# Kernel tuning notes

Measured on AMD Instinct MI355X. Metric: run time of the kernel, lower is better.

## Reference

```python
import jax, jax.numpy as jnp
import numpy as np

P_EPS = 1e-6            # nn.PairwiseDistance default eps
ALPHA = 0.25
STD_TARGET = 1.0
NUM_COMMUNITIES = 512   # C = number of unique community ids
BIG = 1e30              # masking value for hard-negative min


def setup_inputs() -> dict:
    key = jax.random.key(0)
    k1, k2, k3 = jax.random.split(key, 3)
    B, N, D, C = 1, 100000, 128, NUM_COMMUNITIES
    node_features = jax.random.normal(k1, (B, N, D), dtype=jnp.float32)
    # row 0: a permutation of node indices; row 1: community of that node.
    perm = jax.random.permutation(k2, N).astype(jnp.int32)
    comm_per_node = jnp.concatenate([
        jnp.arange(C, dtype=jnp.int32),  # guarantee every community appears
        jax.random.randint(k3, (N - C,), 0, C, dtype=jnp.int32),
    ])
    community_belong_list = jnp.stack([perm, comm_per_node[perm]])  # [2, N]
    return {"node_features": node_features, "community_belong_list": community_belong_list}


def reference(node_features, community_belong_list):
    B, N, D = node_features.shape
    C = NUM_COMMUNITIES
    dt = node_features.dtype

    # ---- _community_inverse_permute: invert row-0 permutation, reorder columns ----
    perm = community_belong_list[0]
    inv = jnp.zeros((N,), perm.dtype).at[perm].add(jnp.arange(N, dtype=perm.dtype))
    cbl = community_belong_list[:, inv]          # row0 == arange(N) after this
    comm = cbl[1]                                # [N] community id per node
    src = node_features[:, cbl[0], :]            # [B,N,D] gather (identity order)

    # ---- groupby sum / count -> community means ----
    comm_sum = jnp.zeros((B, C, D), dt).at[:, comm, :].add(src)        # [B,C,D]
    counts = jnp.zeros((C,), dt).at[comm].add(jnp.asarray(1.0, dt))   # [C]
    comm_mean = comm_sum / counts[None, :, None]                      # [B,C,D]

    # ---- cdist(node_features, comm_mean, p=2) -> [B,N,C] ----
    x2 = jnp.sum(node_features * node_features, -1)                   # [B,N]
    c2 = jnp.sum(comm_mean * comm_mean, -1)                           # [B,C]
    dots = jnp.einsum('bnd,bcd->bnc', node_features, comm_mean)
    distance = jnp.sqrt(jnp.maximum(x2[:, :, None] + c2[:, None, :] - 2.0 * dots, 0.0))

    # ---- leave-one-out community mean per node, positive distance ----
    cnt_pn = counts[comm]                                             # [N]
    cnt_m1 = jnp.maximum(cnt_pn - 1.0, 1.0)                           # [N]
    x_minus = jnp.where((cnt_pn == 1.0)[None, :, None], jnp.asarray(0.0, dt), src)
    loo_mean = (comm_sum[:, comm, :] - x_minus) / cnt_m1[None, :, None]
    pos_dist = jnp.sqrt(jnp.sum((loo_mean - src + P_EPS) ** 2, -1))   # [B,N]

    # ---- negatives: all communities except the node's own ----
    own = distance[:, jnp.arange(N), comm]                            # [B,N]
    mean_neg = (jnp.sum(distance, -1) - own) / (C - 1)                # [B,N]
    pos_mask = jnp.zeros((N, C), bool).at[jnp.arange(N), comm].set(True)
    hard_neg = jnp.min(jnp.where(pos_mask[None], jnp.asarray(BIG, dt), distance), -1)

    trip_mean = jnp.maximum(pos_dist - mean_neg + ALPHA, 0.0)
    trip_min = jnp.maximum(pos_dist - hard_neg + ALPHA, 0.0)

    # ---- groupby std (unbiased) per community per feature ----
    sq = jnp.zeros((B, C, D), dt).at[:, comm, :].add((src - comm_mean[:, comm, :]) ** 2)
    std = jnp.sqrt(sq / jnp.maximum(counts - 1.0, 1.0)[None, :, None])

    return (trip_mean.mean(), trip_min.mean(), ((std - STD_TARGET) ** 2).mean())
```

## Files before the change

### kernel.cpp

```cpp
#include <hip/hip_runtime.h>

#define NCOMM 512
#define DIM   128
#define ALPHA 0.25f
#define PEPS  1e-6f
#define BIGF  1e30f
#define TILE_C 16
#define NT    (NCOMM / TILE_C)

typedef __attribute__((ext_vector_type(8))) short bf16x8;
typedef __attribute__((ext_vector_type(4))) float f32x4;

__device__ __forceinline__ unsigned short bf16_rn(float v) {
    unsigned u = __float_as_uint(v);
    u += 0x7FFFu + ((u >> 16) & 1u);
    return (unsigned short)(u >> 16);
}
__device__ __forceinline__ float bf16_f(unsigned short h) {
    return __uint_as_float((unsigned)h << 16);
}

#define GLOAD_LDS16(g, l) __builtin_amdgcn_global_load_lds( \
    (const __attribute__((address_space(1))) void*)(g), \
    (__attribute__((address_space(3))) void*)(l), 16, 0, 0)


__global__ void k_inv(const int* __restrict__ cbl, int* __restrict__ inv, int N) {
    int i = blockIdx.x * 256 + threadIdx.x;
    if (i < N) inv[cbl[i]] = i;
}

__global__ void k_comm(const int* __restrict__ cbl, const int* __restrict__ inv,
                       int* __restrict__ comm, int* __restrict__ idx0,
                       int* __restrict__ counts, int N) {
    __shared__ int h[NCOMM];
    int t = threadIdx.x;
    h[t] = 0; h[t + 256] = 0;
    __syncthreads();
    int j = blockIdx.x * 256 + t;
    if (j < N) {
        int ij = inv[j];
        int c  = cbl[N + ij];
        comm[j] = c;
        idx0[j] = cbl[ij];
        atomicAdd(&h[c], 1);
    }
    __syncthreads();
    int v = h[t];        if (v) atomicAdd(&counts[t], v);
    v = h[t + 256];      if (v) atomicAdd(&counts[t + 256], v);
}

__global__ void k_scan(const int* __restrict__ counts, int* __restrict__ offsets,
                       int* __restrict__ cursor, float* __restrict__ countf) {
    __shared__ int sc[NCOMM];
    int t = threadIdx.x;
    int v0 = counts[t];
    sc[t] = v0;
    __syncthreads();
    for (int off = 1; off < NCOMM; off <<= 1) {
        int v = (t >= off) ? sc[t - off] : 0;
        __syncthreads();
        sc[t] += v;
        __syncthreads();
    }
    int excl = sc[t] - v0;
    offsets[t] = excl;
    cursor[t]  = excl;
    countf[t]  = (float)v0;
}

__global__ void k_sort(const int* __restrict__ comm, int* __restrict__ cursor,
                       int* __restrict__ sorted, int N) {
    __shared__ int h[NCOMM], hb[NCOMM];
    int t = threadIdx.x;
    h[t] = 0; h[t + 256] = 0;
    __syncthreads();
    int j0 = blockIdx.x * 1024 + t;
    int cs[4];
    #pragma unroll
    for (int q = 0; q < 4; ++q) {
        int j = j0 + q * 256;
        cs[q] = (j < N) ? comm[j] : -1;
        if (cs[q] >= 0) atomicAdd(&h[cs[q]], 1);
    }
    __syncthreads();
    int v = h[t];        if (v) hb[t] = atomicAdd(&cursor[t], v);
    v = h[t + 256];      if (v) hb[t + 256] = atomicAdd(&cursor[t + 256], v);
    __syncthreads();
    #pragma unroll
    for (int q = 0; q < 4; ++q) {
        int j = j0 + q * 256;
        if (cs[q] >= 0) {
            int p = atomicAdd(&hb[cs[q]], 1);
            sorted[p] = j;
        }
    }
}


__global__ void __launch_bounds__(256) k_stats(
        const float* __restrict__ NF, const int* __restrict__ idx0,
        const int* __restrict__ sorted, const int* __restrict__ offsets,
        const int* __restrict__ counts,
        float* __restrict__ comm_sum,
        unsigned short* __restrict__ CMh, unsigned short* __restrict__ CMl,
        float* __restrict__ c2, float* __restrict__ accum) {
    __shared__ int ridx[512];
    __shared__ float4 bufS[256], bufQ[256];
    int c = blockIdx.x, t = threadIdx.x;
    int d4 = t & 31, r = t >> 5;
    int cnt = counts[c], base = offsets[c];
    const float4* NF4 = (const float4*)NF;

    float4 s4 = make_float4(0.f, 0.f, 0.f, 0.f);
    float4 q4 = make_float4(0.f, 0.f, 0.f, 0.f);
    for (int chunk = 0; chunk < cnt; chunk += 512) {
        int m = min(cnt - chunk, 512);
        for (int i = t; i < m; i += 256) ridx[i] = idx0[sorted[base + chunk + i]];
        __syncthreads();
        for (int i = r; i < m; i += 8) {
            float4 v = NF4[(size_t)ridx[i] * 32 + d4];
            s4.x += v.x; s4.y += v.y; s4.z += v.z; s4.w += v.w;
            q4.x = fmaf(v.x, v.x, q4.x); q4.y = fmaf(v.y, v.y, q4.y);
            q4.z = fmaf(v.z, v.z, q4.z); q4.w = fmaf(v.w, v.w, q4.w);
        }
        __syncthreads();
    }
    bufS[t] = s4; bufQ[t] = q4;
    __syncthreads();
    if (t < 128) {
        float4 a = bufS[t], b = bufS[t + 128];
        a.x += b.x; a.y += b.y; a.z += b.z; a.w += b.w; bufS[t] = a;
        float4 e = bufQ[t], f = bufQ[t + 128];
        e.x += f.x; e.y += f.y; e.z += f.z; e.w += f.w; bufQ[t] = e;
    }
    __syncthreads();
    if (t < 64) {
        float4 a = bufS[t], b = bufS[t + 64];
        a.x += b.x; a.y += b.y; a.z += b.z; a.w += b.w; bufS[t] = a;
        float4 e = bufQ[t], f = bufQ[t + 64];
        e.x += f.x; e.y += f.y; e.z += f.z; e.w += f.w; bufQ[t] = e;
    }
    __syncthreads();
    if (t < 32) {
        float4 a = bufS[t], b = bufS[t + 32];
        a.x += b.x; a.y += b.y; a.z += b.z; a.w += b.w;
        float4 e = bufQ[t], f = bufQ[t + 32];
        e.x += f.x; e.y += f.y; e.z += f.z; e.w += f.w;
        float sarr[4] = {a.x, a.y, a.z, a.w};
        float qarr[4] = {e.x, e.y, e.z, e.w};
        float cf = (float)cnt;
        float mm = 0.f, ee = 0.f;
        #pragma unroll
        for (int k = 0; k < 4; ++k) {
            int d = t * 4 + k;
            float s = sarr[k];
            comm_sum[c * DIM + d] = s;
            float m = (cnt > 0) ? s / cf : 0.f;
            unsigned short h = bf16_rn(m);
            CMh[c * DIM + d] = h;
            CMl[c * DIM + d] = bf16_rn(m - bf16_f(h));
            float varn = fmaxf(fmaf(-cf * m, m, qarr[k]), 0.f);
            float stdv = sqrtf(varn / fmaxf(cf - 1.f, 1.f));
            float er = stdv - 1.f;
            mm = fmaf(m, m, mm);
            ee = fmaf(er, er, ee);
        }
        #pragma unroll
        for (int msk = 1; msk < 32; msk <<= 1) {
            mm += __shfl_xor(mm, msk);
            ee += __shfl_xor(ee, msk);
        }
        if (t == 0) {
            c2[c] = mm;
            atomicAdd(&accum[2], ee);
        }
    }
}


__global__ void __launch_bounds__(256, 2) k_main(
        const float* __restrict__ NF,
        const unsigned short* __restrict__ CMh,
        const unsigned short* __restrict__ CMl,
        const float* __restrict__ comm_sum,
        const float* __restrict__ c2g,
        const float* __restrict__ countf,
        const int* __restrict__ comm,
        const int* __restrict__ idx0,
        float* __restrict__ accum, int N) {
    __shared__ unsigned short Bst[4][2][2][TILE_C * DIM];
    __shared__ float c2s[NCOMM];
    __shared__ int   comms[128];
    __shared__ float x2s[128];
    __shared__ float sums[128], mins[128];
    __shared__ float red[8];

    int tid = threadIdx.x;
    int w  = tid >> 6;
    int l  = tid & 63;
    int lr = l & 15;
    int lk = l >> 4;
    int n0 = blockIdx.x * 128;

    auto stage = [&](int tt, int b) {
        int c0 = tt * TILE_C;
        unsigned short* lh = &Bst[w][b][0][0];
        unsigned short* ll = &Bst[w][b][1][0];
        #pragma unroll
        for (int i = 0; i < 4; ++i) {
            int p = i * 64 + l;
            int row = p >> 4, cp = p & 15;
            size_t gch = ((size_t)(c0 + row) * 16 + (cp ^ row)) * 8;
            GLOAD_LDS16(CMh + gch, lh + i * 512);
            GLOAD_LDS16(CMl + gch, ll + i * 512);
        }
    };
    stage(0, 0);

    c2s[tid]       = c2g[tid];
    c2s[tid + 256] = c2g[tid + 256];
    if (tid < 128) {
        int gn = n0 + tid;
        comms[tid] = (gn < N) ? comm[gn] : -1;
    }

    bf16x8 ah[2][4], al[2][4];
    #pragma unroll
    for (int mf = 0; mf < 2; ++mf) {
        int n = n0 + w * 32 + mf * 16 + lr;
        const float4* src = (const float4*)NF + (size_t)n * 32 + lk * 2;
        float p2 = 0.f;
        #pragma unroll
        for (int ks = 0; ks < 4; ++ks) {
            float4 v0 = make_float4(0.f, 0.f, 0.f, 0.f), v1 = v0;
            if (n < N) { v0 = src[ks * 8]; v1 = src[ks * 8 + 1]; }
            float fr[8] = {v0.x, v0.y, v0.z, v0.w, v1.x, v1.y, v1.z, v1.w};
            bf16x8 hh, ll;
            #pragma unroll
            for (int t = 0; t < 8; ++t) {
                unsigned short h = bf16_rn(fr[t]);
                hh[t] = (short)h;
                ll[t] = (short)bf16_rn(fr[t] - bf16_f(h));
                p2 = fmaf(fr[t], fr[t], p2);
            }
            ah[mf][ks] = hh; al[mf][ks] = ll;
        }
        p2 += __shfl_xor(p2, 16);
        p2 += __shfl_xor(p2, 32);
        if (lk == 0) x2s[w * 32 + mf * 16 + lr] = p2;
    }
    __syncthreads();

    float x2v[2][4], sumv[2][4], minv[2][4];
    int cnv[2][4];
    #pragma unroll
    for (int mf = 0; mf < 2; ++mf)
        #pragma unroll
        for (int j = 0; j < 4; ++j) {
            int idx = w * 32 + mf * 16 + lk * 4 + j;
            x2v[mf][j] = x2s[idx];
            cnv[mf][j] = comms[idx];
            sumv[mf][j] = 0.f; minv[mf][j] = BIGF;
        }

    int buf = 0;
    for (int tt = 0; tt < NT; ++tt) {
        if (tt + 1 < NT) {
            stage(tt + 1, buf ^ 1);
            asm volatile("s_waitcnt vmcnt(8)" ::: "memory");
        } else {
            asm volatile("s_waitcnt vmcnt(0)" ::: "memory");
        }
        __builtin_amdgcn_sched_barrier(0);

        const unsigned short* bhp = &Bst[w][buf][0][0];
        const unsigned short* blp = &Bst[w][buf][1][0];
        f32x4 ae0 = {0.f, 0.f, 0.f, 0.f}, ao0 = ae0, ae1 = ae0, ao1 = ae0;
        #pragma unroll
        for (int hf = 0; hf < 2; ++hf) {
            int ke = hf * 2, ko = hf * 2 + 1;
            int che = (ke * 4 + lk) ^ lr;
            int cho = (ko * 4 + lk) ^ lr;
            bf16x8 bhe = *(const bf16x8*)&bhp[(lr * 16 + che) * 8];
            bf16x8 bho = *(const bf16x8*)&bhp[(lr * 16 + cho) * 8];
            bf16x8 ble = *(const bf16x8*)&blp[(lr * 16 + che) * 8];
            bf16x8 blo = *(const bf16x8*)&blp[(lr * 16 + cho) * 8];
            ae0 = __builtin_amdgcn_mfma_f32_16x16x32_bf16(ah[0][ke], bhe, ae0, 0, 0, 0);
            ae1 = __builtin_amdgcn_mfma_f32_16x16x32_bf16(ah[1][ke], bhe, ae1, 0, 0, 0);
            ao0 = __builtin_amdgcn_mfma_f32_16x16x32_bf16(ah[0][ko], bho, ao0, 0, 0, 0);
            ao1 = __builtin_amdgcn_mfma_f32_16x16x32_bf16(ah[1][ko], bho, ao1, 0, 0, 0);
            ae0 = __builtin_amdgcn_mfma_f32_16x16x32_bf16(al[0][ke], bhe, ae0, 0, 0, 0);
            ae1 = __builtin_amdgcn_mfma_f32_16x16x32_bf16(al[1][ke], bhe, ae1, 0, 0, 0);
            ao0 = __builtin_amdgcn_mfma_f32_16x16x32_bf16(al[0][ko], bho, ao0, 0, 0, 0);
            ao1 = __builtin_amdgcn_mfma_f32_16x16x32_bf16(al[1][ko], bho, ao1, 0, 0, 0);
            ae0 = __builtin_amdgcn_mfma_f32_16x16x32_bf16(ah[0][ke], ble, ae0, 0, 0, 0);
            ae1 = __builtin_amdgcn_mfma_f32_16x16x32_bf16(ah[1][ke], ble, ae1, 0, 0, 0);
            ao0 = __builtin_amdgcn_mfma_f32_16x16x32_bf16(ah[0][ko], blo, ao0, 0, 0, 0);
            ao1 = __builtin_amdgcn_mfma_f32_16x16x32_bf16(ah[1][ko], blo, ao1, 0, 0, 0);
        }
        f32x4 acc0 = ae0 + ao0;
        f32x4 acc1 = ae1 + ao1;
        int ccol = tt * TILE_C + lr;
        float c2v = c2s[ccol];
        #pragma unroll
        for (int j = 0; j < 4; ++j) {
            float d2a = fmaf(-2.f, acc0[j], x2v[0][j] + c2v);
            float da  = __builtin_amdgcn_sqrtf(fmaxf(d2a, 0.f));
            sumv[0][j] += da;
            minv[0][j] = fminf(minv[0][j], (cnv[0][j] == ccol) ? BIGF : da);
            float d2b = fmaf(-2.f, acc1[j], x2v[1][j] + c2v);
            float db  = __builtin_amdgcn_sqrtf(fmaxf(d2b, 0.f));
            sumv[1][j] += db;
            minv[1][j] = fminf(minv[1][j], (cnv[1][j] == ccol) ? BIGF : db);
        }
        buf ^= 1;
    }

    #pragma unroll
    for (int mf = 0; mf < 2; ++mf)
        #pragma unroll
        for (int j = 0; j < 4; ++j) {
            float sv = sumv[mf][j], mv = minv[mf][j];
            #pragma unroll
            for (int msk = 1; msk < 16; msk <<= 1) {
                sv += __shfl_xor(sv, msk);
                mv = fminf(mv, __shfl_xor(mv, msk));
            }
            if (lr == 0) {
                int idx = w * 32 + mf * 16 + lk * 4 + j;
                sums[idx] = sv; mins[idx] = mv;
            }
        }
    __syncthreads();

    float tmean = 0.f, tminv = 0.f;
    {
        int ln = tid >> 1, half = tid & 1;
        int n = n0 + ln;
        if (n < N) {
            int cnode = comms[ln];
            float cf  = countf[cnode];
            float cm1 = fmaxf(cf - 1.f, 1.f);
            float rs  = 1.f / cm1;
            bool single = (cf == 1.f);
            const float4* srow = (const float4*)(NF + (size_t)idx0[n] * DIM) + half * 16;
            const float4* csum = (const float4*)(comm_sum + (size_t)cnode * DIM) + half * 16;
            float q = 0.f, dot = 0.f;
            #pragma unroll
            for (int m = 0; m < 16; ++m) {
                float4 sv = srow[m];
                float4 cs = csum[m];
                float4 xm = single ? make_float4(0.f, 0.f, 0.f, 0.f) : sv;
                float lx = (cs.x - xm.x) * rs - sv.x + PEPS;
                float ly = (cs.y - xm.y) * rs - sv.y + PEPS;
                float lz = (cs.z - xm.z) * rs - sv.z + PEPS;
                float lw = (cs.w - xm.w) * rs - sv.w + PEPS;
                q = fmaf(lx, lx, fmaf(ly, ly, fmaf(lz, lz, fmaf(lw, lw, q))));
                dot = fmaf(sv.x, cs.x, fmaf(sv.y, cs.y, fmaf(sv.z, cs.z, fmaf(sv.w, cs.w, dot))));
            }
            q   += __shfl_xor(q, 1);
            dot += __shfl_xor(dot, 1);
            if (half == 0) {
                float pos = sqrtf(q);
                float ownd2 = x2s[ln] + c2s[cnode] - 2.f * (dot / cf);
                float own = sqrtf(fmaxf(ownd2, 0.f));
                float mean_neg = (sums[ln] - own) * (1.f / (float)(NCOMM - 1));
                tmean = fmaxf(pos - mean_neg + ALPHA, 0.f);
                tminv = fmaxf(pos - mins[ln] + ALPHA, 0.f);
            }
        }
    }
    #pragma unroll
    for (int msk = 1; msk < 64; msk <<= 1) {
        tmean += __shfl_xor(tmean, msk);
        tminv += __shfl_xor(tminv, msk);
    }
    if ((tid & 63) == 0) { red[w * 2] = tmean; red[w * 2 + 1] = tminv; }
    __syncthreads();
    if (tid == 0) {
        atomicAdd(&accum[0], red[0] + red[2] + red[4] + red[6]);
        atomicAdd(&accum[1], red[1] + red[3] + red[5] + red[7]);
    }
}

__global__ void k_final(const float* __restrict__ accum, float* __restrict__ out, int N) {
    if (threadIdx.x == 0) {
        out[0] = accum[0] / (float)N;
        out[1] = accum[1] / (float)N;
        out[2] = accum[2] / (float)(NCOMM * DIM);
    }
}


extern "C" void kernel_launch(void* const* d_in, const int* in_sizes, int n_in,
                              void* d_out, int out_size, void* d_ws, size_t ws_size,
                              hipStream_t stream) {
    const float* NF  = (const float*)d_in[0];
    const int*   CBL = (const int*)d_in[1];
    int N = in_sizes[1] / 2;
    if (N <= 0) return;

    char* ws = (char*)d_ws;
    float* accum   = (float*)ws;
    int*   counts  = (int*)(ws + 16);
    int*   cursor  = (int*)(ws + 16 + 2048);
    int*   offsets = (int*)(ws + 16 + 2 * 2048);
    float* countf  = (float*)(ws + 16 + 3 * 2048);
    float* c2      = (float*)(ws + 16 + 4 * 2048);
    char* p = ws + 16 + 5 * 2048;
    int* inv    = (int*)p; p += (size_t)N * 4;
    int* comm   = (int*)p; p += (size_t)N * 4;
    int* idx0   = (int*)p; p += (size_t)N * 4;
    int* sorted = (int*)p; p += (size_t)N * 4;
    float* comm_sum = (float*)p; p += (size_t)NCOMM * DIM * 4;
    unsigned short* CMh = (unsigned short*)p; p += (size_t)NCOMM * DIM * 2;
    unsigned short* CMl = (unsigned short*)p;

    hipMemsetAsync(d_ws, 0, 16 + 2048, stream);

    int nb = (N + 255) / 256;
    k_inv <<<nb, 256, 0, stream>>>(CBL, inv, N);
    k_comm<<<nb, 256, 0, stream>>>(CBL, inv, comm, idx0, counts, N);
    k_scan<<<1, NCOMM, 0, stream>>>(counts, offsets, cursor, countf);
    int nb4 = (N + 1023) / 1024;
    k_sort<<<nb4, 256, 0, stream>>>(comm, cursor, sorted, N);
    k_stats<<<NCOMM, 256, 0, stream>>>(NF, idx0, sorted, offsets, counts,
                                       comm_sum, CMh, CMl, c2, accum);
    int mb = (N + 127) / 128;
    k_main<<<mb, 256, 0, stream>>>(NF, CMh, CMl, comm_sum, c2, countf,
                                   comm, idx0, accum, N);
    k_final<<<1, 64, 0, stream>>>(accum, (float*)d_out, N);
}
```

Baseline: 147.3 us.

## Split community dimension across two blocks with shared LDS staging and a separate triplet reduction

k_main now splits the 512 communities into two halves, each handled by its own block, which doubles the grid. Partial sums and mins go to global buffers, and a new k_trip kernel combines them and reduces the triplet losses. The B tiles are now shared by all four waves through one double-buffered LDS tile of 32 communities, with __syncthreads, instead of each wave keeping its own copy. This cuts LDS use and lets launch bounds rise to 4 blocks per SM for more occupancy. The cost is the node A-fragments being loaded and converted twice, extra global traffic and a kernel launch, and added block-wide barriers.

After: 223.8 us. 1.52x slower.

```diff
diff --git a/kernel.cpp b/kernel.cpp
--- a/kernel.cpp
+++ b/kernel.cpp
@@ -5,8 +5,7 @@
 #define ALPHA 0.25f
 #define PEPS  1e-6f
 #define BIGF  1e30f
-#define TILE_C 16
-#define NT    (NCOMM / TILE_C)
+#define TILE_C 32
 
 typedef __attribute__((ext_vector_type(8))) short bf16x8;
 typedef __attribute__((ext_vector_type(4))) float f32x4;
@@ -179,7 +178,7 @@
 }
 
 
-__global__ void __launch_bounds__(256, 2) k_main(
+__global__ void __launch_bounds__(256, 4) k_main(
         const float* __restrict__ NF,
         const unsigned short* __restrict__ CMh,
         const unsigned short* __restrict__ CMl,
@@ -188,38 +187,47 @@
         const float* __restrict__ countf,
         const int* __restrict__ comm,
         const int* __restrict__ idx0,
-        float* __restrict__ accum, int N) {
-    __shared__ unsigned short Bst[4][2][2][TILE_C * DIM];
-    __shared__ float c2s[NCOMM];
+        float* __restrict__ sp, float* __restrict__ mp,
+        float* __restrict__ pos_g, float* __restrict__ own_g,
+        int N, int RB) {
+    __shared__ unsigned short Bst[2][2][TILE_C * DIM];
+    __shared__ float c2s[256];
     __shared__ int   comms[128];
     __shared__ float x2s[128];
     __shared__ float sums[128], mins[128];
-    __shared__ float red[8];
 
     int tid = threadIdx.x;
+    int bid = blockIdx.x;
+    int ch  = (bid >= RB) ? 1 : 0;
+    int rb  = bid - ch * RB;
     int w  = tid >> 6;
     int l  = tid & 63;
     int lr = l & 15;
     int lk = l >> 4;
-    int n0 = blockIdx.x * 128;
-
-    auto stage = [&](int tt, int b) {
-        int c0 = tt * TILE_C;
-        unsigned short* lh = &Bst[w][b][0][0];
-        unsigned short* ll = &Bst[w][b][1][0];
-        #pragma unroll
-        for (int i = 0; i < 4; ++i) {
-            int p = i * 64 + l;
-            int row = p >> 4, cp = p & 15;
-            size_t gch = ((size_t)(c0 + row) * 16 + (cp ^ row)) * 8;
-            GLOAD_LDS16(CMh + gch, lh + i * 512);
-            GLOAD_LDS16(CMl + gch, ll + i * 512);
-        }
+    int n0 = rb * 128;
+    int c0 = ch * 256;
+    int NP = RB * 128;
+
+    const unsigned short* pH0; const unsigned short* pH1;
+    const unsigned short* pL0; const unsigned short* pL1;
+    {
+        int r0 = tid >> 4;
+        int s0 = (tid & 15) ^ (r0 & 15);
+        pH0 = CMh + ((size_t)(c0 + r0) * 16 + s0) * 8;
+        pH1 = CMh + ((size_t)(c0 + 16 + r0) * 16 + s0) * 8;
+        pL0 = CMl + ((size_t)(c0 + r0) * 16 + s0) * 8;
+        pL1 = CMl + ((size_t)(c0 + 16 + r0) * 16 + s0) * 8;
+    }
+    auto stage = [&](int b) {
+        GLOAD_LDS16(pH0, &Bst[b][0][(size_t)(0 * 256 + w * 64) * 8]);
+        GLOAD_LDS16(pH1, &Bst[b][0][(size_t)(1 * 256 + w * 64) * 8]);
+        GLOAD_LDS16(pL0, &Bst[b][1][(size_t)(0 * 256 + w * 64) * 8]);
+        GLOAD_LDS16(pL1, &Bst[b][1][(size_t)(1 * 256 + w * 64) * 8]);
+        pH0 += 4096; pH1 += 4096; pL0 += 4096; pL1 += 4096;
     };
-    stage(0, 0);
-
-    c2s[tid]       = c2g[tid];
-    c2s[tid + 256] = c2g[tid + 256];
+    stage(0);
+
+    c2s[tid] = c2g[c0 + tid];
     if (tid < 128) {
         int gn = n0 + tid;
         comms[tid] = (gn < N) ? comm[gn] : -1;
@@ -265,55 +273,55 @@
         }
 
     int buf = 0;
-    for (int tt = 0; tt < NT; ++tt) {
-        if (tt + 1 < NT) {
-            stage(tt + 1, buf ^ 1);
-            asm volatile("s_waitcnt vmcnt(8)" ::: "memory");
-        } else {
-            asm volatile("s_waitcnt vmcnt(0)" ::: "memory");
-        }
-        __builtin_amdgcn_sched_barrier(0);
-
-        const unsigned short* bhp = &Bst[w][buf][0][0];
-        const unsigned short* blp = &Bst[w][buf][1][0];
-        f32x4 ae0 = {0.f, 0.f, 0.f, 0.f}, ao0 = ae0, ae1 = ae0, ao1 = ae0;
-        #pragma unroll
-        for (int hf = 0; hf < 2; ++hf) {
-            int ke = hf * 2, ko = hf * 2 + 1;
-            int che = (ke * 4 + lk) ^ lr;
-            int cho = (ko * 4 + lk) ^ lr;
-            bf16x8 bhe = *(const bf16x8*)&bhp[(lr * 16 + che) * 8];
-            bf16x8 bho = *(const bf16x8*)&bhp[(lr * 16 + cho) * 8];
-            bf16x8 ble = *(const bf16x8*)&blp[(lr * 16 + che) * 8];
-            bf16x8 blo = *(const bf16x8*)&blp[(lr * 16 + cho) * 8];
-            ae0 = __builtin_amdgcn_mfma_f32_16x16x32_bf16(ah[0][ke], bhe, ae0, 0, 0, 0);
-            ae1 = __builtin_amdgcn_mfma_f32_16x16x32_bf16(ah[1][ke], bhe, ae1, 0, 0, 0);
-            ao0 = __builtin_amdgcn_mfma_f32_16x16x32_bf16(ah[0][ko], bho, ao0, 0, 0, 0);
-            ao1 = __builtin_amdgcn_mfma_f32_16x16x32_bf16(ah[1][ko], bho, ao1, 0, 0, 0);
-            ae0 = __builtin_amdgcn_mfma_f32_16x16x32_bf16(al[0][ke], bhe, ae0, 0, 0, 0);
-            ae1 = __builtin_amdgcn_mfma_f32_16x16x32_bf16(al[1][ke], bhe, ae1, 0, 0, 0);
-            ao0 = __builtin_amdgcn_mfma_f32_16x16x32_bf16(al[0][ko], bho, ao0, 0, 0, 0);
-            ao1 = __builtin_amdgcn_mfma_f32_16x16x32_bf16(al[1][ko], bho, ao1, 0, 0, 0);
-            ae0 = __builtin_amdgcn_mfma_f32_16x16x32_bf16(ah[0][ke], ble, ae0, 0, 0, 0);
-            ae1 = __builtin_amdgcn_mfma_f32_16x16x32_bf16(ah[1][ke], ble, ae1, 0, 0, 0);
-            ao0 = __builtin_amdgcn_mfma_f32_16x16x32_bf16(ah[0][ko], blo, ao0, 0, 0, 0);
-            ao1 = __builtin_amdgcn_mfma_f32_16x16x32_bf16(ah[1][ko], blo, ao1, 0, 0, 0);
-        }
-        f32x4 acc0 = ae0 + ao0;
-        f32x4 acc1 = ae1 + ao1;
-        int ccol = tt * TILE_C + lr;
-        float c2v = c2s[ccol];
-        #pragma unroll
-        for (int j = 0; j < 4; ++j) {
-            float d2a = fmaf(-2.f, acc0[j], x2v[0][j] + c2v);
-            float da  = __builtin_amdgcn_sqrtf(fmaxf(d2a, 0.f));
-            sumv[0][j] += da;
-            minv[0][j] = fminf(minv[0][j], (cnv[0][j] == ccol) ? BIGF : da);
-            float d2b = fmaf(-2.f, acc1[j], x2v[1][j] + c2v);
-            float db  = __builtin_amdgcn_sqrtf(fmaxf(d2b, 0.f));
-            sumv[1][j] += db;
-            minv[1][j] = fminf(minv[1][j], (cnv[1][j] == ccol) ? BIGF : db);
-        }
+    for (int tt = 0; tt < 8; ++tt) {
+        if (tt < 7) stage(buf ^ 1);
+
+        #pragma unroll
+        for (int s = 0; s < 2; ++s) {
+            int rbase = s * 16 + lr;
+            const unsigned short* bhp = &Bst[buf][0][0];
+            const unsigned short* blp = &Bst[buf][1][0];
+            f32x4 ae0 = {0.f, 0.f, 0.f, 0.f}, ao0 = ae0, ae1 = ae0, ao1 = ae0;
+            #pragma unroll
+            for (int hf = 0; hf < 2; ++hf) {
+                int ke = hf * 2, ko = hf * 2 + 1;
+                int che = (ke * 4 + lk) ^ lr;
+                int cho = (ko * 4 + lk) ^ lr;
+                bf16x8 bhe = *(const bf16x8*)&bhp[(size_t)(rbase * 16 + che) * 8];
+                bf16x8 bho = *(const bf16x8*)&bhp[(size_t)(rbase * 16 + cho) * 8];
+                bf16x8 ble = *(const bf16x8*)&blp[(size_t)(rbase * 16 + che) * 8];
+                bf16x8 blo = *(const bf16x8*)&blp[(size_t)(rbase * 16 + cho) * 8];
+                ae0 = __builtin_amdgcn_mfma_f32_16x16x32_bf16(ah[0][ke], bhe, ae0, 0, 0, 0);
+                ae1 = __builtin_amdgcn_mfma_f32_16x16x32_bf16(ah[1][ke], bhe, ae1, 0, 0, 0);
+                ao0 = __builtin_amdgcn_mfma_f32_16x16x32_bf16(ah[0][ko], bho, ao0, 0, 0, 0);
+                ao1 = __builtin_amdgcn_mfma_f32_16x16x32_bf16(ah[1][ko], bho, ao1, 0, 0, 0);
+                ae0 = __builtin_amdgcn_mfma_f32_16x16x32_bf16(al[0][ke], bhe, ae0, 0, 0, 0);
+                ae1 = __builtin_amdgcn_mfma_f32_16x16x32_bf16(al[1][ke], bhe, ae1, 0, 0, 0);
+                ao0 = __builtin_amdgcn_mfma_f32_16x16x32_bf16(al[0][ko], bho, ao0, 0, 0, 0);
+                ao1 = __builtin_amdgcn_mfma_f32_16x16x32_bf16(al[1][ko], bho, ao1, 0, 0, 0);
+                ae0 = __builtin_amdgcn_mfma_f32_16x16x32_bf16(ah[0][ke], ble, ae0, 0, 0, 0);
+                ae1 = __builtin_amdgcn_mfma_f32_16x16x32_bf16(ah[1][ke], ble, ae1, 0, 0, 0);
+                ao0 = __builtin_amdgcn_mfma_f32_16x16x32_bf16(ah[0][ko], blo, ao0, 0, 0, 0);
+                ao1 = __builtin_amdgcn_mfma_f32_16x16x32_bf16(ah[1][ko], blo, ao1, 0, 0, 0);
+            }
+            f32x4 acc0 = ae0 + ao0;
+            f32x4 acc1 = ae1 + ao1;
+            int ccl = tt * TILE_C + s * 16 + lr;
+            int ccol = c0 + ccl;
+            float c2v = c2s[ccl];
+            #pragma unroll
+            for (int j = 0; j < 4; ++j) {
+                float d2a = fmaf(-2.f, acc0[j], x2v[0][j] + c2v);
+                float da  = __builtin_amdgcn_sqrtf(fmaxf(d2a, 0.f));
+                sumv[0][j] += da;
+                minv[0][j] = fminf(minv[0][j], (cnv[0][j] == ccol) ? BIGF : da);
+                float d2b = fmaf(-2.f, acc1[j], x2v[1][j] + c2v);
+                float db  = __builtin_amdgcn_sqrtf(fmaxf(d2b, 0.f));
+                sumv[1][j] += db;
+                minv[1][j] = fminf(minv[1][j], (cnv[1][j] == ccol) ? BIGF : db);
+            }
+        }
+        __syncthreads();
         buf ^= 1;
     }
 
@@ -334,8 +342,13 @@
         }
     __syncthreads();
 
-    float tmean = 0.f, tminv = 0.f;
-    {
+    if (tid < 128) {
+        int n = n0 + tid;
+        sp[(size_t)ch * NP + n] = sums[tid];
+        mp[(size_t)ch * NP + n] = mins[tid];
+    }
+
+    if (ch == 0) {
         int ln = tid >> 1, half = tid & 1;
         int n = n0 + ln;
         if (n < N) {
@@ -362,23 +375,39 @@
             q   += __shfl_xor(q, 1);
             dot += __shfl_xor(dot, 1);
             if (half == 0) {
-                float pos = sqrtf(q);
-                float ownd2 = x2s[ln] + c2s[cnode] - 2.f * (dot / cf);
-                float own = sqrtf(fmaxf(ownd2, 0.f));
-                float mean_neg = (sums[ln] - own) * (1.f / (float)(NCOMM - 1));
-                tmean = fmaxf(pos - mean_neg + ALPHA, 0.f);
-                tminv = fmaxf(pos - mins[ln] + ALPHA, 0.f);
-            }
-        }
+                pos_g[n] = sqrtf(q);
+                float ownd2 = x2s[ln] + c2g[cnode] - 2.f * (dot / cf);
+                own_g[n] = sqrtf(fmaxf(ownd2, 0.f));
+            }
+        }
+    }
+}
+
+
+__global__ void __launch_bounds__(256) k_trip(
+        const float* __restrict__ sp, const float* __restrict__ mp,
+        const float* __restrict__ pos_g, const float* __restrict__ own_g,
+        float* __restrict__ accum, int N, int NP) {
+    __shared__ float red[8];
+    int i = blockIdx.x * 256 + threadIdx.x;
+    float tm = 0.f, tn = 0.f;
+    if (i < N) {
+        float own = own_g[i];
+        float sum = sp[i] + sp[(size_t)NP + i] - own;
+        float mn  = fminf(mp[i], mp[(size_t)NP + i]);
+        float pos = pos_g[i];
+        tm = fmaxf(pos - sum * (1.f / (float)(NCOMM - 1)) + ALPHA, 0.f);
+        tn = fmaxf(pos - mn + ALPHA, 0.f);
     }
     #pragma unroll
     for (int msk = 1; msk < 64; msk <<= 1) {
-        tmean += __shfl_xor(tmean, msk);
-        tminv += __shfl_xor(tminv, msk);
-    }
-    if ((tid & 63) == 0) { red[w * 2] = tmean; red[w * 2 + 1] = tminv; }
-    __syncthreads();
-    if (tid == 0) {
+        tm += __shfl_xor(tm, msk);
+        tn += __shfl_xor(tn, msk);
+    }
+    int wv = threadIdx.x >> 6;
+    if ((threadIdx.x & 63) == 0) { red[wv * 2] = tm; red[wv * 2 + 1] = tn; }
+    __syncthreads();
+    if (threadIdx.x == 0) {
         atomicAdd(&accum[0], red[0] + red[2] + red[4] + red[6]);
         atomicAdd(&accum[1], red[1] + red[3] + red[5] + red[7]);
     }
@@ -400,6 +429,8 @@
     const int*   CBL = (const int*)d_in[1];
     int N = in_sizes[1] / 2;
     if (N <= 0) return;
+    int RB = (N + 127) / 128;
+    int NP = RB * 128;
 
     char* ws = (char*)d_ws;
     float* accum   = (float*)ws;
@@ -415,7 +446,11 @@
     int* sorted = (int*)p; p += (size_t)N * 4;
     float* comm_sum = (float*)p; p += (size_t)NCOMM * DIM * 4;
     unsigned short* CMh = (unsigned short*)p; p += (size_t)NCOMM * DIM * 2;
-    unsigned short* CMl = (unsigned short*)p;
+    unsigned short* CMl = (unsigned short*)p; p += (size_t)NCOMM * DIM * 2;
+    float* sp    = (float*)p; p += (size_t)2 * NP * 4;
+    float* mp    = (float*)p; p += (size_t)2 * NP * 4;
+    float* pos_g = (float*)p; p += (size_t)NP * 4;
+    float* own_g = (float*)p;
 
     hipMemsetAsync(d_ws, 0, 16 + 2048, stream);
 
@@ -427,8 +462,8 @@
     k_sort<<<nb4, 256, 0, stream>>>(comm, cursor, sorted, N);
     k_stats<<<NCOMM, 256, 0, stream>>>(NF, idx0, sorted, offsets, counts,
                                        comm_sum, CMh, CMl, c2, accum);
-    int mb = (N + 127) / 128;
-    k_main<<<mb, 256, 0, stream>>>(NF, CMh, CMl, comm_sum, c2, countf,
-                                   comm, idx0, accum, N);
+    k_main<<<2 * RB, 256, 0, stream>>>(NF, CMh, CMl, comm_sum, c2, countf,
+                                       comm, idx0, sp, mp, pos_g, own_g, N, RB);
+    k_trip<<<(N + 255) / 256, 256, 0, stream>>>(sp, mp, pos_g, own_g, accum, N, NP);
     k_final<<<1, 64, 0, stream>>>(accum, (float*)d_out, N);
 }
```

## Process 256 nodes per block and seed MFMA accumulators with x2 term

Applied to the files above, without the earlier changes.

Each wave now handles 64 node rows (four 16-row fragments) instead of 32, so every staged community tile in LDS is reused across twice as many MFMAs. Accumulators start at -0.5*|x|^2, which folds the x2 add into the matrix multiply, and the global staging offsets are precomputed once. The epilogue now uses one thread per node instead of two. The cost is higher register pressure from the larger A fragments and accumulators, and half as many blocks, which could hurt occupancy and load balance.

Measured after the change: 148.4 us. No clear change (+0.8%).

```diff
diff --git a/kernel.cpp b/kernel.cpp
--- a/kernel.cpp
+++ b/kernel.cpp
@@ -191,9 +191,9 @@
         float* __restrict__ accum, int N) {
     __shared__ unsigned short Bst[4][2][2][TILE_C * DIM];
     __shared__ float c2s[NCOMM];
-    __shared__ int   comms[128];
-    __shared__ float x2s[128];
-    __shared__ float sums[128], mins[128];
+    __shared__ int   comms[256];
+    __shared__ float x2s[256];
+    __shared__ float sums[256], mins[256];
     __shared__ float red[8];
 
     int tid = threadIdx.x;
@@ -201,34 +201,38 @@
     int l  = tid & 63;
     int lr = l & 15;
     int lk = l >> 4;
-    int n0 = blockIdx.x * 128;
-
+    int n0 = blockIdx.x * 256;
+
+    int goff[4];
+    #pragma unroll
+    for (int i = 0; i < 4; ++i) {
+        int p = i * 64 + l;
+        int row = p >> 4, cp = p & 15;
+        goff[i] = (row * 16 + (cp ^ row)) * 8;
+    }
     auto stage = [&](int tt, int b) {
-        int c0 = tt * TILE_C;
+        int base = tt * (TILE_C * DIM);
         unsigned short* lh = &Bst[w][b][0][0];
         unsigned short* ll = &Bst[w][b][1][0];
         #pragma unroll
         for (int i = 0; i < 4; ++i) {
-            int p = i * 64 + l;
-            int row = p >> 4, cp = p & 15;
-            size_t gch = ((size_t)(c0 + row) * 16 + (cp ^ row)) * 8;
-            GLOAD_LDS16(CMh + gch, lh + i * 512);
-            GLOAD_LDS16(CMl + gch, ll + i * 512);
+            GLOAD_LDS16(CMh + base + goff[i], lh + i * 512);
+            GLOAD_LDS16(CMl + base + goff[i], ll + i * 512);
         }
     };
     stage(0, 0);
 
     c2s[tid]       = c2g[tid];
     c2s[tid + 256] = c2g[tid + 256];
-    if (tid < 128) {
+    {
         int gn = n0 + tid;
         comms[tid] = (gn < N) ? comm[gn] : -1;
     }
 
-    bf16x8 ah[2][4], al[2][4];
-    #pragma unroll
-    for (int mf = 0; mf < 2; ++mf) {
-        int n = n0 + w * 32 + mf * 16 + lr;
+    bf16x8 ah[4][4], al[4][4];
+    #pragma unroll
+    for (int mf = 0; mf < 4; ++mf) {
+        int n = n0 + w * 64 + mf * 16 + lr;
         const float4* src = (const float4*)NF + (size_t)n * 32 + lk * 2;
         float p2 = 0.f;
         #pragma unroll
@@ -248,19 +252,17 @@
         }
         p2 += __shfl_xor(p2, 16);
         p2 += __shfl_xor(p2, 32);
-        if (lk == 0) x2s[w * 32 + mf * 16 + lr] = p2;
-    }
-    __syncthreads();
-
-    float x2v[2][4], sumv[2][4], minv[2][4];
-    int cnv[2][4];
-    #pragma unroll
-    for (int mf = 0; mf < 2; ++mf)
+        if (lk == 0) x2s[w * 64 + mf * 16 + lr] = -0.5f * p2;
+    }
+    __syncthreads();
+
+    int cnv[4][4];
+    float sumv[4][4], minv[4][4];
+    #pragma unroll
+    for (int mf = 0; mf < 4; ++mf)
         #pragma unroll
         for (int j = 0; j < 4; ++j) {
-            int idx = w * 32 + mf * 16 + lk * 4 + j;
-            x2v[mf][j] = x2s[idx];
-            cnv[mf][j] = comms[idx];
+            cnv[mf][j] = comms[w * 64 + mf * 16 + lk * 4 + j];
             sumv[mf][j] = 0.f; minv[mf][j] = BIGF;
         }
 
@@ -276,49 +278,47 @@
 
         const unsigned short* bhp = &Bst[w][buf][0][0];
         const unsigned short* blp = &Bst[w][buf][1][0];
-        f32x4 ae0 = {0.f, 0.f, 0.f, 0.f}, ao0 = ae0, ae1 = ae0, ao1 = ae0;
-        #pragma unroll
-        for (int hf = 0; hf < 2; ++hf) {
-            int ke = hf * 2, ko = hf * 2 + 1;
-            int che = (ke * 4 + lk) ^ lr;
-            int cho = (ko * 4 + lk) ^ lr;
-            bf16x8 bhe = *(const bf16x8*)&bhp[(lr * 16 + che) * 8];
-            bf16x8 bho = *(const bf16x8*)&bhp[(lr * 16 + cho) * 8];
-            bf16x8 ble = *(const bf16x8*)&blp[(lr * 16 + che) * 8];
-            bf16x8 blo = *(const bf16x8*)&blp[(lr * 16 + cho) * 8];
-            ae0 = __builtin_amdgcn_mfma_f32_16x16x32_bf16(ah[0][ke], bhe, ae0, 0, 0, 0);
-            ae1 = __builtin_amdgcn_mfma_f32_16x16x32_bf16(ah[1][ke], bhe, ae1, 0, 0, 0);
-            ao0 = __builtin_amdgcn_mfma_f32_16x16x32_bf16(ah[0][ko], bho, ao0, 0, 0, 0);
-            ao1 = __builtin_amdgcn_mfma_f32_16x16x32_bf16(ah[1][ko], bho, ao1, 0, 0, 0);
-            ae0 = __builtin_amdgcn_mfma_f32_16x16x32_bf16(al[0][ke], bhe, ae0, 0, 0, 0);
-            ae1 = __builtin_amdgcn_mfma_f32_16x16x32_bf16(al[1][ke], bhe, ae1, 0, 0, 0);
-            ao0 = __builtin_amdgcn_mfma_f32_16x16x32_bf16(al[0][ko], bho, ao0, 0, 0, 0);
-            ao1 = __builtin_amdgcn_mfma_f32_16x16x32_bf16(al[1][ko], bho, ao1, 0, 0, 0);
-            ae0 = __builtin_amdgcn_mfma_f32_16x16x32_bf16(ah[0][ke], ble, ae0, 0, 0, 0);
-            ae1 = __builtin_amdgcn_mfma_f32_16x16x32_bf16(ah[1][ke], ble, ae1, 0, 0, 0);
-            ao0 = __builtin_amdgcn_mfma_f32_16x16x32_bf16(ah[0][ko], blo, ao0, 0, 0, 0);
-            ao1 = __builtin_amdgcn_mfma_f32_16x16x32_bf16(ah[1][ko], blo, ao1, 0, 0, 0);
-        }
-        f32x4 acc0 = ae0 + ao0;
-        f32x4 acc1 = ae1 + ao1;
+        bf16x8 bh[4], bl[4];
+        #pragma unroll
+        for (int ks = 0; ks < 4; ++ks) {
+            int ch = (ks * 4 + lk) ^ lr;
+            bh[ks] = *(const bf16x8*)&bhp[(size_t)(lr * 16 + ch) * 8];
+            bl[ks] = *(const bf16x8*)&blp[(size_t)(lr * 16 + ch) * 8];
+        }
+        f32x4 acc[4];
+        #pragma unroll
+        for (int mf = 0; mf < 4; ++mf)
+            acc[mf] = *(const f32x4*)&x2s[w * 64 + mf * 16 + lk * 4];
+
+        #pragma unroll
+        for (int ks = 0; ks < 4; ++ks) {
+            #pragma unroll
+            for (int mf = 0; mf < 4; ++mf)
+                acc[mf] = __builtin_amdgcn_mfma_f32_16x16x32_bf16(ah[mf][ks], bh[ks], acc[mf], 0, 0, 0);
+            #pragma unroll
+            for (int mf = 0; mf < 4; ++mf)
+                acc[mf] = __builtin_amdgcn_mfma_f32_16x16x32_bf16(al[mf][ks], bh[ks], acc[mf], 0, 0, 0);
+            #pragma unroll
+            for (int mf = 0; mf < 4; ++mf)
+                acc[mf] = __builtin_amdgcn_mfma_f32_16x16x32_bf16(ah[mf][ks], bl[ks], acc[mf], 0, 0, 0);
+        }
+
         int ccol = tt * TILE_C + lr;
         float c2v = c2s[ccol];
         #pragma unroll
-        for (int j = 0; j < 4; ++j) {
-            float d2a = fmaf(-2.f, acc0[j], x2v[0][j] + c2v);
-            float da  = __builtin_amdgcn_sqrtf(fmaxf(d2a, 0.f));
-            sumv[0][j] += da;
-            minv[0][j] = fminf(minv[0][j], (cnv[0][j] == ccol) ? BIGF : da);
-            float d2b = fmaf(-2.f, acc1[j], x2v[1][j] + c2v);
-            float db  = __builtin_amdgcn_sqrtf(fmaxf(d2b, 0.f));
-            sumv[1][j] += db;
-            minv[1][j] = fminf(minv[1][j], (cnv[1][j] == ccol) ? BIGF : db);
-        }
+        for (int mf = 0; mf < 4; ++mf)
+            #pragma unroll
+            for (int j = 0; j < 4; ++j) {
+                float d2 = fmaf(-2.f, acc[mf][j], c2v);
+                float da = __builtin_amdgcn_sqrtf(fmaxf(d2, 0.f));
+                sumv[mf][j] += da;
+                minv[mf][j] = fminf(minv[mf][j], (cnv[mf][j] == ccol) ? BIGF : da);
+            }
         buf ^= 1;
     }
 
     #pragma unroll
-    for (int mf = 0; mf < 2; ++mf)
+    for (int mf = 0; mf < 4; ++mf)
         #pragma unroll
         for (int j = 0; j < 4; ++j) {
             float sv = sumv[mf][j], mv = minv[mf][j];
@@ -328,7 +328,7 @@
                 mv = fminf(mv, __shfl_xor(mv, msk));
             }
             if (lr == 0) {
-                int idx = w * 32 + mf * 16 + lk * 4 + j;
+                int idx = w * 64 + mf * 16 + lk * 4 + j;
                 sums[idx] = sv; mins[idx] = mv;
             }
         }
@@ -336,7 +336,7 @@
 
     float tmean = 0.f, tminv = 0.f;
     {
-        int ln = tid >> 1, half = tid & 1;
+        int ln = tid;
         int n = n0 + ln;
         if (n < N) {
             int cnode = comms[ln];
@@ -344,11 +344,11 @@
             float cm1 = fmaxf(cf - 1.f, 1.f);
             float rs  = 1.f / cm1;
             bool single = (cf == 1.f);
-            const float4* srow = (const float4*)(NF + (size_t)idx0[n] * DIM) + half * 16;
-            const float4* csum = (const float4*)(comm_sum + (size_t)cnode * DIM) + half * 16;
+            const float4* srow = (const float4*)(NF + (size_t)idx0[n] * DIM);
+            const float4* csum = (const float4*)(comm_sum + (size_t)cnode * DIM);
             float q = 0.f, dot = 0.f;
-            #pragma unroll
-            for (int m = 0; m < 16; ++m) {
+            #pragma unroll 8
+            for (int m = 0; m < 32; ++m) {
                 float4 sv = srow[m];
                 float4 cs = csum[m];
                 float4 xm = single ? make_float4(0.f, 0.f, 0.f, 0.f) : sv;
@@ -359,16 +359,13 @@
                 q = fmaf(lx, lx, fmaf(ly, ly, fmaf(lz, lz, fmaf(lw, lw, q))));
                 dot = fmaf(sv.x, cs.x, fmaf(sv.y, cs.y, fmaf(sv.z, cs.z, fmaf(sv.w, cs.w, dot))));
             }
-            q   += __shfl_xor(q, 1);
-            dot += __shfl_xor(dot, 1);
-            if (half == 0) {
-                float pos = sqrtf(q);
-                float ownd2 = x2s[ln] + c2s[cnode] - 2.f * (dot / cf);
-                float own = sqrtf(fmaxf(ownd2, 0.f));
-                float mean_neg = (sums[ln] - own) * (1.f / (float)(NCOMM - 1));
-                tmean = fmaxf(pos - mean_neg + ALPHA, 0.f);
-                tminv = fmaxf(pos - mins[ln] + ALPHA, 0.f);
-            }
+            float pos = sqrtf(q);
+            float x2 = -2.f * x2s[ln];
+            float ownd2 = x2 + c2s[cnode] - 2.f * (dot / cf);
+            float own = sqrtf(fmaxf(ownd2, 0.f));
+            float mean_neg = (sums[ln] - own) * (1.f / (float)(NCOMM - 1));
+            tmean = fmaxf(pos - mean_neg + ALPHA, 0.f);
+            tminv = fmaxf(pos - mins[ln] + ALPHA, 0.f);
         }
     }
     #pragma unroll
@@ -427,7 +424,7 @@
     k_sort<<<nb4, 256, 0, stream>>>(comm, cursor, sorted, N);
     k_stats<<<NCOMM, 256, 0, stream>>>(NF, idx0, sorted, offsets, counts,
                                        comm_sum, CMh, CMl, c2, accum);
-    int mb = (N + 127) / 128;
+    int mb = (N + 255) / 256;
     k_main<<<mb, 256, 0, stream>>>(NF, CMh, CMl, comm_sum, c2, countf,
                                    comm, idx0, accum, N);
     k_final<<<1, 64, 0, stream>>>(accum, (float*)d_out, N);
```
